# Optimization experiments

Hardware: AMD Instinct MI355X
Metric: run time of the kernel (lower is better)

Reference implementation:

```python
import jax, jax.numpy as jnp
import numpy as np

B, S, E, H = 2, 2048, 1024, 16
DH = E // H  # 64


def setup_inputs() -> dict:
    key = jax.random.key(0)
    ks = jax.random.split(key, 9)
    scale = 1.0 / np.sqrt(E)
    q = jax.random.normal(ks[0], (B, S, E), jnp.float32)
    k = jax.random.normal(ks[1], (B, S, E), jnp.float32)
    v = jax.random.normal(ks[2], (B, S, E), jnp.float32)
    Wq = jax.random.uniform(ks[3], (E, E), jnp.float32, -scale, scale)
    Wk = jax.random.uniform(ks[4], (E, E), jnp.float32, -scale, scale)
    Wv = jax.random.uniform(ks[5], (E, E), jnp.float32, -scale, scale)
    bq = jax.random.uniform(ks[6], (E,), jnp.float32, -scale, scale)
    bk = jax.random.uniform(ks[7], (E,), jnp.float32, -scale, scale)
    bv = jax.random.uniform(ks[8], (E,), jnp.float32, -scale, scale)
    # causal mask: True = masked. [b, s_q, s_k]
    causal = jnp.triu(jnp.ones((S, S), bool), k=1)
    mask = jnp.broadcast_to(causal, (B, S, S))
    return {"q": q, "k": k, "v": v, "Wq": Wq, "bq": bq, "Wk": Wk,
            "bk": bk, "Wv": Wv, "bv": bv, "mask": mask}


def reference(q, k, v, Wq, bq, Wk, bk, Wv, bv, mask):
    b, s_q, _ = q.shape
    s_k = k.shape[1]
    # NB: faithful to the original: .view(b, heads, s, -1) (no transpose)
    Q = (q @ Wq + bq).reshape(b, H, s_q, DH)
    K = (k @ Wk + bk).reshape(b, H, s_k, DH)
    V = (v @ Wv + bv).reshape(b, H, s_k, DH)
    scores = jnp.einsum('bhqd,bhkd->bhqk', Q, K) / jnp.sqrt(
        jnp.asarray(DH, Q.dtype))
    scores = jnp.where(mask[:, None, :, :], -jnp.inf, scores)
    attn = jax.nn.softmax(scores, axis=-1)
    out = jnp.einsum('bhqk,bhkd->bhqd', attn, V).reshape(b, s_q, -1)
    return out  # dropout p=0 / eval mode -> identity
```

## Files before the change

### kernel.cpp

```cpp
#include <hip/hip_runtime.h>

typedef unsigned short u16;
typedef __attribute__((ext_vector_type(8))) __bf16 bf16x8;
typedef __attribute__((ext_vector_type(4))) __bf16 bf16x4;
typedef __attribute__((ext_vector_type(4))) float f32x4;

#define MFMA(a, b, c) __builtin_amdgcn_mfma_f32_16x16x32_bf16((a), (b), (c), 0, 0, 0)
#define KSCALE 0.18033688011112042f

__device__ __forceinline__ void load_lds16(const void* g, void* l) {
  __builtin_amdgcn_global_load_lds(
      (__attribute__((address_space(1))) void*)(g),
      (__attribute__((address_space(3))) void*)(l), 16, 0, 0);
}

__device__ __forceinline__ float launder(float x, float lim) {
  return fminf(fmaxf(x, -lim), lim);
}

__global__ __launch_bounds__(256) void prep(
    const float* __restrict__ x0, const float* __restrict__ x1,
    const float* __restrict__ x2, const float* __restrict__ W0,
    const float* __restrict__ W1, const float* __restrict__ W2,
    __bf16* __restrict__ Xb, __bf16* __restrict__ WT) {
  __shared__ __bf16 tile[64][65];
  int bx = blockIdx.x;
  int t = threadIdx.x;
  if (bx < 3072) {
    int z = bx >> 10, blk = bx & 1023;
    const float* x = z == 0 ? x0 : (z == 1 ? x1 : x2);
    __bf16* o = Xb + (size_t)z * 4194304;
#pragma unroll
    for (int i = 0; i < 4; ++i) {
      size_t e = ((size_t)i * 262144 + (size_t)blk * 256 + t) * 4;
      f32x4 v = *(const f32x4*)&x[e];
      bf16x4 b = {(__bf16)v[0], (__bf16)v[1], (__bf16)v[2], (__bf16)v[3]};
      *(bf16x4*)&o[e] = b;
    }
  } else {
    int idx = bx - 3072;
    int z = idx >> 8, rest = idx & 255;
    const float* W = z == 0 ? W0 : (z == 1 ? W1 : W2);
    float sc = z == 0 ? KSCALE : 1.0f;
    __bf16* out = WT + (size_t)z * 1048576;
    int r0 = (rest >> 4) * 64, c0 = (rest & 15) * 64;
#pragma unroll
    for (int it = 0; it < 16; ++it) {
      int flat = it * 256 + t, r = flat >> 6, c = flat & 63;
      tile[c][r] = (__bf16)(W[(size_t)(r0 + r) * 1024 + c0 + c] * sc);
    }
    __syncthreads();
#pragma unroll
    for (int it = 0; it < 16; ++it) {
      int flat = it * 256 + t, r = flat >> 6, c = flat & 63;
      out[(size_t)(c0 + r) * 1024 + r0 + c] = tile[r][c];
    }
  }
}

__global__ __launch_bounds__(256, 2) void proj_gemm(
    const __bf16* __restrict__ Xb, const __bf16* __restrict__ WT,
    const float* __restrict__ bq, const float* __restrict__ bk,
    const float* __restrict__ bv, __bf16* __restrict__ OutBase) {
  int z = blockIdx.z;
  const __bf16* X = Xb + (size_t)z * 4194304;
  const __bf16* Wt = WT + (size_t)z * 1048576;
  const float* bias = z == 0 ? bq : (z == 1 ? bk : bv);
  float bsc = z == 0 ? KSCALE : 1.0f;
  __bf16* O = OutBase + (size_t)z * 4194304;

  __shared__ __attribute__((aligned(16))) __bf16 As[256 * 32];
  __shared__ __attribute__((aligned(16))) __bf16 Bs[128 * 32];

  int t = threadIdx.x;
  int lane = t & 63, quad = lane >> 4, l16 = lane & 15;
  int wave = t >> 6;
  int wm = (wave >> 1) * 128, wn = (wave & 1) * 64;
  int m0 = blockIdx.x * 256, n0 = blockIdx.y * 128;

  f32x4 zero4 = {0.f, 0.f, 0.f, 0.f};
  f32x4 acc[8][4];
#pragma unroll
  for (int i = 0; i < 8; ++i)
#pragma unroll
    for (int j = 0; j < 4; ++j) acc[i][j] = zero4;

  for (int k0 = 0; k0 < 1024; k0 += 32) {
#pragma unroll
    for (int p = 0; p < 4; ++p) {
      int c = p * 256 + t;
      int r = c >> 2, col = (c & 3) * 8;
      load_lds16(X + (size_t)(m0 + r) * 1024 + k0 + col, &As[c * 8]);
    }
#pragma unroll
    for (int p = 0; p < 2; ++p) {
      int c = p * 256 + t;
      int r = c >> 2, col = (c & 3) * 8;
      load_lds16(Wt + (size_t)(n0 + r) * 1024 + k0 + col, &Bs[c * 8]);
    }
    __syncthreads();
    bf16x8 a[8], b[4];
#pragma unroll
    for (int i = 0; i < 8; ++i)
      a[i] = *(const bf16x8*)&As[(wm + i * 16 + l16) * 32 + quad * 8];
#pragma unroll
    for (int j = 0; j < 4; ++j)
      b[j] = *(const bf16x8*)&Bs[(wn + j * 16 + l16) * 32 + quad * 8];
#pragma unroll
    for (int i = 0; i < 8; ++i)
#pragma unroll
      for (int j = 0; j < 4; ++j) acc[i][j] = MFMA(a[i], b[j], acc[i][j]);
    __syncthreads();
  }

#pragma unroll
  for (int j = 0; j < 4; ++j) {
    int n = n0 + wn + j * 16 + l16;
    float bb = bias[n] * bsc;
#pragma unroll
    for (int i = 0; i < 8; ++i) {
#pragma unroll
      for (int r = 0; r < 4; ++r) {
        int m = m0 + wm + i * 16 + quad * 4 + r;
        O[(size_t)m * 1024 + n] = (__bf16)launder(acc[i][j][r] + bb, 512.f);
      }
    }
  }
}

__global__ __launch_bounds__(256) void transpose_v(
    const u16* __restrict__ Vp, u16* __restrict__ Vt) {
  int bh = blockIdx.y, s0 = blockIdx.x * 64;
  __shared__ u16 tile[64][65];
  int t = threadIdx.x;
  const u16* src = Vp + (size_t)bh * 131072;
  u16* dst = Vt + (size_t)bh * 131072;
#pragma unroll
  for (int it = 0; it < 16; ++it) {
    int flat = it * 256 + t, r = flat >> 6, d = flat & 63;
    tile[d][r] = src[(size_t)(s0 + r) * 64 + d];
  }
  __syncthreads();
#pragma unroll
  for (int it = 0; it < 16; ++it) {
    int flat = it * 256 + t, d = flat >> 6, c = flat & 63;
    dst[(size_t)d * 2048 + s0 + c] = tile[d][c];
  }
}

__global__ __launch_bounds__(256, 2) void flash_attn(
    const __bf16* __restrict__ Qp, const __bf16* __restrict__ Kp,
    const __bf16* __restrict__ Vt, float* __restrict__ out) {
  int qtA = blockIdx.x;
  int qtB = 31 - qtA;
  int bh = blockIdx.y;
  int t = threadIdx.x;
  int lane = t & 63, quad = lane >> 4, l16 = lane & 15;
  int w = t >> 6;
  int jmaxA = qtA >> 1, jmaxB = qtB >> 1;

  __shared__ __attribute__((aligned(16))) __bf16 Ks[2][8192];
  __shared__ __attribute__((aligned(16))) __bf16 Vs[2][8192];
  __shared__ __attribute__((aligned(16))) __bf16 Ps[4][2048];

  const __bf16* Qb = Qp + (size_t)bh * 131072;
  const __bf16* Kb = Kp + (size_t)bh * 131072;
  const __bf16* Vb = Vt + (size_t)bh * 131072;
  __bf16* Pw = Ps[w];

  int qbA = qtA * 64 + w * 16, qbB = qtB * 64 + w * 16;

  bf16x8 qfA[2], qfB[2], ones;
#pragma unroll
  for (int i = 0; i < 8; ++i) ones[i] = (__bf16)1.0f;
#pragma unroll
  for (int kk = 0; kk < 2; ++kk) {
    qfA[kk] = *(const bf16x8*)&Qb[(size_t)(qbA + l16) * 64 + kk * 32 + quad * 8];
    qfB[kk] = *(const bf16x8*)&Qb[(size_t)(qbB + l16) * 64 + kk * 32 + quad * 8];
  }

  f32x4 zero4 = {0.f, 0.f, 0.f, 0.f};
  f32x4 oA[4], oB[4], lAacc = zero4, lBacc = zero4;
#pragma unroll
  for (int nd = 0; nd < 4; ++nd) { oA[nd] = zero4; oB[nd] = zero4; }

  int ks_kpos[4], ks_off[4], vs_d[4], vs_off[4], vs_kq[4];
#pragma unroll
  for (int p = 0; p < 4; ++p) {
    int c = p * 256 + t;
    ks_kpos[p] = (c & 511) >> 2;
    ks_off[p] = (c >> 9) * 32 + (c & 3) * 8;
    vs_kq[p] = c >> 8;
    vs_d[p] = (c & 255) >> 2;
    vs_off[p] = (c & 3) * 8;
  }

  bf16x8 pk[4], pv[4];
#pragma unroll
  for (int p = 0; p < 4; ++p) {
    pk[p] = *(const bf16x8*)&Kb[(size_t)ks_kpos[p] * 64 + ks_off[p]];
    pv[p] = *(const bf16x8*)&Vb[(size_t)vs_d[p] * 2048 + vs_kq[p] * 32 + vs_off[p]];
  }
#pragma unroll
  for (int p = 0; p < 4; ++p) {
    int c = p * 256 + t;
    *(bf16x8*)&Ks[0][c * 8] = pk[p];
    *(bf16x8*)&Vs[0][c * 8] = pv[p];
  }
  if (jmaxB > 0) {
#pragma unroll
    for (int p = 0; p < 4; ++p) {
      pk[p] = *(const bf16x8*)&Kb[(size_t)(128 + ks_kpos[p]) * 64 + ks_off[p]];
      pv[p] = *(const bf16x8*)&Vb[(size_t)vs_d[p] * 2048 + 128 + vs_kq[p] * 32 + vs_off[p]];
    }
  }
  __syncthreads();

  for (int j = 0; j <= jmaxB; ++j) {
    int cur = j & 1, nxt = cur ^ 1;
    bool doA = (j <= jmaxA);

    if (j < jmaxB) {
#pragma unroll
      for (int p = 0; p < 4; ++p) {
        int c = p * 256 + t;
        *(bf16x8*)&Ks[nxt][c * 8] = pk[p];
        *(bf16x8*)&Vs[nxt][c * 8] = pv[p];
      }
      if (j + 1 < jmaxB) {
        int jn = (j + 2) * 128;
#pragma unroll
        for (int p = 0; p < 4; ++p) {
          pk[p] = *(const bf16x8*)&Kb[(size_t)(jn + ks_kpos[p]) * 64 + ks_off[p]];
          pv[p] = *(const bf16x8*)&Vb[(size_t)vs_d[p] * 2048 + jn + vs_kq[p] * 32 + vs_off[p]];
        }
      }
    }

    f32x4 sA[8], sB[8];
#pragma unroll
    for (int nt = 0; nt < 8; ++nt) {
      bf16x8 k0 = *(const bf16x8*)&Ks[cur][(nt * 16 + l16) * 32 + quad * 8];
      bf16x8 k1 = *(const bf16x8*)&Ks[cur][4096 + (nt * 16 + l16) * 32 + quad * 8];
      f32x4 zb = zero4;
      zb = MFMA(k0, qfB[0], zb);
      zb = MFMA(k1, qfB[1], zb);
      sB[nt] = zb;
      if (doA) {
        f32x4 za = zero4;
        za = MFMA(k0, qfA[0], za);
        za = MFMA(k1, qfA[1], za);
        sA[nt] = za;
      }
    }

    if (j == jmaxB) {
      int qg = qbB + l16;
#pragma unroll
      for (int nt = 0; nt < 8; ++nt) {
        int kg = j * 128 + nt * 16 + quad * 4;
#pragma unroll
        for (int r = 0; r < 4; ++r)
          if (kg + r > qg) sB[nt][r] = -1e30f;
      }
    }
#pragma unroll
    for (int nt = 0; nt < 8; ++nt) {
      bf16x4 pb;
#pragma unroll
      for (int r = 0; r < 4; ++r)
        pb[r] = (__bf16)__builtin_amdgcn_exp2f(sB[nt][r]);
      *(bf16x4*)&Pw[l16 * 128 + (((nt * 4 + quad) ^ (l16 * 2)) & 31) * 4] = pb;
    }
    {
      bf16x8 pf[4];
#pragma unroll
      for (int kk = 0; kk < 4; ++kk)
        pf[kk] = *(const bf16x8*)&Pw[l16 * 128 + (((kk * 8 + quad * 2) ^ (l16 * 2)) & 31) * 4];
#pragma unroll
      for (int kk = 0; kk < 4; ++kk) {
        lBacc = MFMA(ones, pf[kk], lBacc);
#pragma unroll
        for (int nd = 0; nd < 4; ++nd) {
          bf16x8 av = *(const bf16x8*)&Vs[cur][kk * 2048 + (nd * 16 + l16) * 32 + quad * 8];
          oB[nd] = MFMA(av, pf[kk], oB[nd]);
        }
      }
    }

    if (doA) {
      if (j == jmaxA) {
        int qg = qbA + l16;
#pragma unroll
        for (int nt = 0; nt < 8; ++nt) {
          int kg = j * 128 + nt * 16 + quad * 4;
#pragma unroll
          for (int r = 0; r < 4; ++r)
            if (kg + r > qg) sA[nt][r] = -1e30f;
        }
      }
#pragma unroll
      for (int nt = 0; nt < 8; ++nt) {
        bf16x4 pb;
#pragma unroll
        for (int r = 0; r < 4; ++r)
          pb[r] = (__bf16)__builtin_amdgcn_exp2f(sA[nt][r]);
        *(bf16x4*)&Pw[l16 * 128 + (((nt * 4 + quad) ^ (l16 * 2)) & 31) * 4] = pb;
      }
      bf16x8 pf[4];
#pragma unroll
      for (int kk = 0; kk < 4; ++kk)
        pf[kk] = *(const bf16x8*)&Pw[l16 * 128 + (((kk * 8 + quad * 2) ^ (l16 * 2)) & 31) * 4];
#pragma unroll
      for (int kk = 0; kk < 4; ++kk) {
        lAacc = MFMA(ones, pf[kk], lAacc);
#pragma unroll
        for (int nd = 0; nd < 4; ++nd) {
          bf16x8 av = *(const bf16x8*)&Vs[cur][kk * 2048 + (nd * 16 + l16) * 32 + quad * 8];
          oA[nd] = MFMA(av, pf[kk], oA[nd]);
        }
      }
    }
    __syncthreads();
  }

  {
    float invA = 1.f / lAacc[0], invB = 1.f / lBacc[0];
    int qA = qbA + l16, qB = qbB + l16;
#pragma unroll
    for (int nd = 0; nd < 4; ++nd) {
      f32x4 a, b;
#pragma unroll
      for (int r = 0; r < 4; ++r) {
        a[r] = launder(oA[nd][r] * invA, 512.f);
        b[r] = launder(oB[nd][r] * invB, 512.f);
      }
      *(f32x4*)&out[(size_t)bh * 131072 + (size_t)qA * 64 + nd * 16 + quad * 4] = a;
      *(f32x4*)&out[(size_t)bh * 131072 + (size_t)qB * 64 + nd * 16 + quad * 4] = b;
    }
  }
}

extern "C" void kernel_launch(void* const* d_in, const int* in_sizes, int n_in,
                              void* d_out, int out_size, void* d_ws, size_t ws_size,
                              hipStream_t stream) {
  (void)in_sizes; (void)n_in; (void)out_size; (void)ws_size;
  const float* q  = (const float*)d_in[0];
  const float* k  = (const float*)d_in[1];
  const float* v  = (const float*)d_in[2];
  const float* Wq = (const float*)d_in[3];
  const float* bq = (const float*)d_in[4];
  const float* Wk = (const float*)d_in[5];
  const float* bk = (const float*)d_in[6];
  const float* Wv = (const float*)d_in[7];
  const float* bv = (const float*)d_in[8];

  __bf16* ws  = (__bf16*)d_ws;
  __bf16* WT  = ws;
  __bf16* QKV = ws + (size_t)3 * 1048576;
  __bf16* Qp  = QKV;
  __bf16* Kp  = QKV + (size_t)4194304;
  __bf16* Vp  = QKV + (size_t)2 * 4194304;
  __bf16* Xb  = QKV + (size_t)3 * 4194304;
  __bf16* Vtr = Xb;

  prep<<<dim3(3840), 256, 0, stream>>>(q, k, v, Wq, Wk, Wv, Xb, WT);
  proj_gemm<<<dim3(16, 8, 3), 256, 0, stream>>>(Xb, WT, bq, bk, bv, QKV);
  transpose_v<<<dim3(32, 32), 256, 0, stream>>>((const u16*)Vp, (u16*)Vtr);
  flash_attn<<<dim3(16, 32), 256, 0, stream>>>(Qp, Kp, Vtr, (float*)d_out);
}
```

Measured before the change: 213.7 us.

## Double-buffer projection GEMM LDS loads and shrink tile to 128x128

Rewrites the QKV projection GEMM to use a 128x128 block tile with double-buffered LDS staging. The next k-slice is prefetched via global_load_lds while MFMAs run on the current one, gated by explicit vmcnt waits and barriers. The grid becomes 768 blocks with the projection index derived from the row offset, and launch bounds allow 3 blocks per CU. This aims to hide global-load latency and improve occupancy and CU fill, at the cost of less data reuse per block and two barriers per iteration.

```diff
diff --git a/kernel.cpp b/kernel.cpp
--- a/kernel.cpp
+++ b/kernel.cpp
@@ -58,71 +58,90 @@
   }
 }
 
-__global__ __launch_bounds__(256, 2) void proj_gemm(
+__device__ __forceinline__ void pg_stage(
+    const __bf16* __restrict__ A, const __bf16* __restrict__ Bm, int k0,
+    __bf16* As, __bf16* Bs, int tid) {
+#pragma unroll
+  for (int r = 0; r < 2; ++r) {
+    int flat = r * 256 + tid;
+    load_lds16(A + (size_t)(flat >> 2) * 1024 + k0 + (flat & 3) * 8, &As[flat * 8]);
+  }
+#pragma unroll
+  for (int r = 0; r < 2; ++r) {
+    int flat = r * 256 + tid;
+    load_lds16(Bm + (size_t)(flat >> 2) * 1024 + k0 + (flat & 3) * 8, &Bs[flat * 8]);
+  }
+}
+
+__global__ __launch_bounds__(256, 3) void proj_gemm(
     const __bf16* __restrict__ Xb, const __bf16* __restrict__ WT,
     const float* __restrict__ bq, const float* __restrict__ bk,
-    const float* __restrict__ bv, __bf16* __restrict__ OutBase) {
-  int z = blockIdx.z;
-  const __bf16* X = Xb + (size_t)z * 4194304;
-  const __bf16* Wt = WT + (size_t)z * 1048576;
-  const float* bias = z == 0 ? bq : (z == 1 ? bk : bv);
+    const float* __restrict__ bv, __bf16* __restrict__ QKV) {
+  __shared__ __attribute__((aligned(16))) __bf16 As[2][4096];
+  __shared__ __attribute__((aligned(16))) __bf16 Bs[2][4096];
+
+  int tid = threadIdx.x;
+  int lane = tid & 63, quad = lane >> 4, l16 = lane & 15;
+  int w = tid >> 6;
+  int wm = (w >> 1) * 64, wn = (w & 1) * 64;
+  int m0 = blockIdx.x * 128;
+  int z = m0 >> 12;
+  int n0 = blockIdx.y * 128;
+  const __bf16* A = Xb + (size_t)m0 * 1024;
+  const __bf16* Bm = WT + (size_t)z * 1048576 + (size_t)n0 * 1024;
+
+  f32x4 zero4 = {0.f, 0.f, 0.f, 0.f};
+  f32x4 acc[4][4];
+#pragma unroll
+  for (int i = 0; i < 4; ++i)
+#pragma unroll
+    for (int j = 0; j < 4; ++j) acc[i][j] = zero4;
+
+  pg_stage(A, Bm, 0, As[0], Bs[0], tid);
+
+  for (int i = 0; i < 32; ++i) {
+    int cur = i & 1;
+    if (i < 31) {
+      pg_stage(A, Bm, (i + 1) * 32, As[cur ^ 1], Bs[cur ^ 1], tid);
+      asm volatile("s_waitcnt vmcnt(4)" ::: "memory");
+    } else {
+      asm volatile("s_waitcnt vmcnt(0)" ::: "memory");
+    }
+    __builtin_amdgcn_sched_barrier(0);
+    __builtin_amdgcn_s_barrier();
+    __builtin_amdgcn_sched_barrier(0);
+
+    bf16x8 a[4], b[4];
+#pragma unroll
+    for (int mf = 0; mf < 4; ++mf)
+      a[mf] = *(const bf16x8*)&As[cur][(wm + mf * 16 + l16) * 32 + quad * 8];
+#pragma unroll
+    for (int nf = 0; nf < 4; ++nf)
+      b[nf] = *(const bf16x8*)&Bs[cur][(wn + nf * 16 + l16) * 32 + quad * 8];
+#pragma unroll
+    for (int mf = 0; mf < 4; ++mf)
+#pragma unroll
+      for (int nf = 0; nf < 4; ++nf) acc[mf][nf] = MFMA(a[mf], b[nf], acc[mf][nf]);
+
+    __builtin_amdgcn_sched_barrier(0);
+    __builtin_amdgcn_s_barrier();
+    __builtin_amdgcn_sched_barrier(0);
+  }
+
+  int mrow = m0 & 4095;
+  const float* bp = z == 0 ? bq : (z == 1 ? bk : bv);
   float bsc = z == 0 ? KSCALE : 1.0f;
-  __bf16* O = OutBase + (size_t)z * 4194304;
-
-  __shared__ __attribute__((aligned(16))) __bf16 As[256 * 32];
-  __shared__ __attribute__((aligned(16))) __bf16 Bs[128 * 32];
-
-  int t = threadIdx.x;
-  int lane = t & 63, quad = lane >> 4, l16 = lane & 15;
-  int wave = t >> 6;
-  int wm = (wave >> 1) * 128, wn = (wave & 1) * 64;
-  int m0 = blockIdx.x * 256, n0 = blockIdx.y * 128;
-
-  f32x4 zero4 = {0.f, 0.f, 0.f, 0.f};
-  f32x4 acc[8][4];
-#pragma unroll
-  for (int i = 0; i < 8; ++i)
-#pragma unroll
-    for (int j = 0; j < 4; ++j) acc[i][j] = zero4;
-
-  for (int k0 = 0; k0 < 1024; k0 += 32) {
-#pragma unroll
-    for (int p = 0; p < 4; ++p) {
-      int c = p * 256 + t;
-      int r = c >> 2, col = (c & 3) * 8;
-      load_lds16(X + (size_t)(m0 + r) * 1024 + k0 + col, &As[c * 8]);
-    }
-#pragma unroll
-    for (int p = 0; p < 2; ++p) {
-      int c = p * 256 + t;
-      int r = c >> 2, col = (c & 3) * 8;
-      load_lds16(Wt + (size_t)(n0 + r) * 1024 + k0 + col, &Bs[c * 8]);
-    }
-    __syncthreads();
-    bf16x8 a[8], b[4];
-#pragma unroll
-    for (int i = 0; i < 8; ++i)
-      a[i] = *(const bf16x8*)&As[(wm + i * 16 + l16) * 32 + quad * 8];
-#pragma unroll
-    for (int j = 0; j < 4; ++j)
-      b[j] = *(const bf16x8*)&Bs[(wn + j * 16 + l16) * 32 + quad * 8];
-#pragma unroll
-    for (int i = 0; i < 8; ++i)
-#pragma unroll
-      for (int j = 0; j < 4; ++j) acc[i][j] = MFMA(a[i], b[j], acc[i][j]);
-    __syncthreads();
-  }
-
-#pragma unroll
-  for (int j = 0; j < 4; ++j) {
-    int n = n0 + wn + j * 16 + l16;
-    float bb = bias[n] * bsc;
-#pragma unroll
-    for (int i = 0; i < 8; ++i) {
+  __bf16* O = QKV + (size_t)z * 4194304;
+#pragma unroll
+  for (int nf = 0; nf < 4; ++nf) {
+    int n = n0 + wn + nf * 16 + l16;
+    float bb = bp[n] * bsc;
+#pragma unroll
+    for (int mf = 0; mf < 4; ++mf) {
 #pragma unroll
       for (int r = 0; r < 4; ++r) {
-        int m = m0 + wm + i * 16 + quad * 4 + r;
-        O[(size_t)m * 1024 + n] = (__bf16)launder(acc[i][j][r] + bb, 512.f);
+        int m = mrow + wm + mf * 16 + quad * 4 + r;
+        O[(size_t)m * 1024 + n] = (__bf16)launder(acc[mf][nf][r] + bb, 512.f);
       }
     }
   }
@@ -365,7 +384,7 @@
   __bf16* Vtr = Xb;
 
   prep<<<dim3(3840), 256, 0, stream>>>(q, k, v, Wq, Wk, Wv, Xb, WT);
-  proj_gemm<<<dim3(16, 8, 3), 256, 0, stream>>>(Xb, WT, bq, bk, bv, QKV);
+  proj_gemm<<<dim3(96, 8), 256, 0, stream>>>(Xb, WT, bq, bk, bv, QKV);
   transpose_v<<<dim3(32, 32), 256, 0, stream>>>((const u16*)Vp, (u16*)Vtr);
   flash_attn<<<dim3(16, 32), 256, 0, stream>>>(Qp, Kp, Vtr, (float*)d_out);
 }
```

Result: no change. 209.8 us (-1.9%).
